# Kernel tuning notes

Measured on AMD Instinct MI355X. Metric: run time of the kernel, lower is better.

## Reference

```python
import jax, jax.numpy as jnp
import numpy as np

B, S, D, K = 32, 1024, 256, 1024
DECAY = 0.99
EPS = 1e-05          # EMA laplace epsilon
LN_EPS = 1e-05       # LayerNorm epsilon
COMMITMENT_COST = 0.25


def setup_inputs() -> dict:
    key = jax.random.key(0)
    k1, k2, k3 = jax.random.split(key, 3)
    inputs = jax.random.normal(k1, (B, S, D), jnp.float32)
    # nn.Embedding init: uniform(-1/K, 1/K)
    weight = jax.random.uniform(k2, (K, D), jnp.float32, -1.0 / K, 1.0 / K)
    ema_w = jax.random.normal(k3, (K, D), jnp.float32)
    ema_cluster_size = jnp.zeros((K,), jnp.float32)
    ln_gamma = jnp.ones((D,), jnp.float32)
    ln_beta = jnp.zeros((D,), jnp.float32)
    return {"inputs": inputs, "weight": weight, "ema_w": ema_w,
            "ema_cluster_size": ema_cluster_size,
            "ln_gamma": ln_gamma, "ln_beta": ln_beta}


def _layernorm(x, g, b):
    mu = jnp.mean(x, axis=-1, keepdims=True)
    var = jnp.mean((x - mu) ** 2, axis=-1, keepdims=True)
    return (x - mu) * jax.lax.rsqrt(var + LN_EPS) * g + b


def reference(inputs, weight, ema_w, ema_cluster_size, ln_gamma, ln_beta):
    flat_input = inputs.reshape(-1, D)          # [N, D] (unnormalized, used for EMA dw)
    feats = _layernorm(flat_input, ln_gamma, ln_beta)  # norm_input in sample()

    # euclidean distances ||f||^2 + ||w||^2 - 2 f w^T  -> [N, K]
    d = (jnp.sum(feats ** 2, axis=1, keepdims=True)
         + jnp.sum(weight ** 2, axis=1)
         - 2.0 * feats @ weight.T)

    sampled_dist = jnp.min(d, axis=1)           # [N]
    idx_flat = jnp.argmin(d, axis=1)            # [N] int

    # faithful reproduction of the source's reordering:
    # argsort per batch row (values in [0,S)) then flat-index into the [N]-long index vector
    order = jnp.argsort(sampled_dist.reshape(B, S), axis=1).reshape(-1)  # [N], values in [0,S)
    enc_idx = idx_flat[order]                   # [N]

    quantized = weight[enc_idx].reshape(B, S, D)

    # ---- EMA codebook update (training path), no gradients ----
    fi = jax.lax.stop_gradient(flat_input)
    counts = jax.ops.segment_sum(jnp.ones((B * S,), jnp.float32), enc_idx,
                                 num_segments=K)                    # encodings.sum(0)
    new_cs = ema_cluster_size * DECAY + (1.0 - DECAY) * counts
    n = jnp.sum(new_cs)
    new_cs = (new_cs + EPS) / (n + K * EPS) * n
    dw = jax.ops.segment_sum(fi, enc_idx, num_segments=K)            # encodings.T @ flat_input
    new_ema_w = jax.lax.stop_gradient(ema_w) * DECAY + (1.0 - DECAY) * dw
    new_weight = new_ema_w / new_cs[:, None]

    # ---- losses (avg=False, loss_type=0) ----
    e_latent = jnp.mean((jax.lax.stop_gradient(quantized) - inputs) ** 2)
    q_latent = jnp.mean((quantized - jax.lax.stop_gradient(inputs)) ** 2)
    loss = q_latent + COMMITMENT_COST * e_latent

    # straight-through estimator
    quantized_st = inputs + jax.lax.stop_gradient(quantized - inputs)

    avg_probs = counts / (B * S)
    perplexity = jnp.exp(-jnp.sum(avg_probs * jnp.log(avg_probs + 1e-10)))

    return quantized_st, loss, perplexity, enc_idx, new_weight, new_ema_w, new_cs
```

## Files before the change

### kernel.cpp

```cpp
#include <hip/hip_runtime.h>
#include <cmath>

#define B_ 32
#define S_ 1024
#define D_ 256
#define K_ 1024
#define N_ (B_*S_)

#define O_Q     0
#define O_LOSS  8388608
#define O_PERP  8388609
#define O_IDX   8388610
#define O_NW    8421378
#define O_NEW   8683522
#define O_NCS   8945666

#define OFF_FH    0ull
#define OFF_WH    16777216ull
#define OFF_BW    17301504ull
#define OFF_BWF   17309696ull
#define OFF_SAMP  17313792ull
#define OFF_IDXF  17575936ull
#define OFF_ENC   17707008ull
#define OFF_CNT   17838080ull
#define OFF_SLOWC 17842176ull
#define OFF_SLOWL 17842240ull
#define OFF_LOSSP 17973312ull
#define OFF_COFF  18235456ull
#define OFF_CUR   18239552ull
#define OFF_ROWL  18243648ull

#define MARGIN 4e-5f

typedef _Float16 f16x8 __attribute__((ext_vector_type(8)));
typedef float    f32x4 __attribute__((ext_vector_type(4)));

#define GL16(gp, lp) __builtin_amdgcn_global_load_lds( \
    (const __attribute__((address_space(1))) unsigned int*)(const void*)(gp), \
    (__attribute__((address_space(3))) unsigned int*)(void*)(lp), 16, 0, 0)

__global__ void k_pre(const float* __restrict__ x, const float* __restrict__ gam,
                      const float* __restrict__ bet, _Float16* __restrict__ fh,
                      const float* __restrict__ w, double* __restrict__ Bw,
                      float* __restrict__ Bwf, _Float16* __restrict__ wh) {
    int lane = threadIdx.x & 63, wv = threadIdx.x >> 6;
    if (blockIdx.x < N_ / 4) {
        int n = blockIdx.x * 4 + wv;
        const float* row = x + (size_t)n * D_;
        double xv[4], gv[4], bv[4];
#pragma unroll
        for (int i = 0; i < 4; i++) {
            int d = lane + 64 * i;
            xv[i] = row[d]; gv[i] = gam[d]; bv[i] = bet[d];
        }
        double s = xv[0] + xv[1] + xv[2] + xv[3];
        for (int m = 32; m > 0; m >>= 1) s += __shfl_xor(s, m, 64);
        double mu = s / 256.0, vs = 0.0;
#pragma unroll
        for (int i = 0; i < 4; i++) { double c = xv[i] - mu; vs += c * c; }
        for (int m = 32; m > 0; m >>= 1) vs += __shfl_xor(vs, m, 64);
        double inv = 1.0 / sqrt(vs / 256.0 + 1e-5);
#pragma unroll
        for (int i = 0; i < 4; i++) {
            int d = lane + 64 * i;
            float ff = (float)((xv[i] - mu) * inv * gv[i] + bv[i]);
            fh[(size_t)n * D_ + d] = (_Float16)ff;
        }
    } else {
        int k = (blockIdx.x - N_ / 4) * 4 + wv;
        double s = 0.0;
#pragma unroll
        for (int i = 0; i < 4; i++) {
            int d = lane + 64 * i;
            float v = w[(size_t)k * D_ + d];
            s += (double)v * (double)v;
            wh[(size_t)k * D_ + d] = (_Float16)v;
        }
        for (int m = 32; m > 0; m >>= 1) s += __shfl_xor(s, m, 64);
        if (lane == 0) { Bw[k] = s; Bwf[k] = (float)s; }
    }
}

__launch_bounds__(512, 4)
__global__ void k_phase1(const _Float16* __restrict__ fh, const _Float16* __restrict__ wh,
                         const float* __restrict__ Bwf, float* __restrict__ pq) {
    __shared__ __align__(16) _Float16 sA[3][128][32];
    __shared__ __align__(16) _Float16 sB[3][256][32];

    const int tid = threadIdx.x;
    const int lane = tid & 63;
    const int w = tid >> 6;
    const int wr = w >> 2;
    const int wc = w & 3;
    const int l15 = lane & 15;
    const int g = lane >> 4;
    const int id = blockIdx.x;
    const int grp = (id & 7) * 32 + (id >> 5);
    const int chunk = (id >> 3) & 3;
    const int row0 = grp * 128;
    const int c0 = chunk * 256;

    const int srow = lane >> 2;
    const int scol = (lane & 3) * 8;
    const _Float16* gp[3];
    int lrow[3]; int isA[3];
#pragma unroll
    for (int j = 0; j < 3; j++) {
        int li = w * 3 + j;
        if (li < 8) {
            isA[j] = 1; lrow[j] = li * 16;
            gp[j] = fh + (size_t)(row0 + li * 16 + srow) * 256 + scol;
        } else {
            isA[j] = 0; lrow[j] = (li - 8) * 16;
            gp[j] = wh + (size_t)(c0 + (li - 8) * 16 + srow) * 256 + scol;
        }
    }

    f32x4 acc[4][4];
#pragma unroll
    for (int a = 0; a < 4; a++)
#pragma unroll
        for (int b = 0; b < 4; b++) acc[a][b] = (f32x4){0.f, 0.f, 0.f, 0.f};

#define STAGE(bi, kk) do { \
    const int eoff_ = (kk) * 32; \
    _Pragma("unroll") \
    for (int j_ = 0; j_ < 3; j_++) { \
        if (isA[j_]) GL16(gp[j_] + eoff_, &sA[bi][lrow[j_]][0]); \
        else         GL16(gp[j_] + eoff_, &sB[bi][lrow[j_]][0]); \
    } \
} while (0)

    STAGE(0, 0);
    STAGE(1, 1);
    asm volatile("s_waitcnt vmcnt(3)" ::: "memory");
    __builtin_amdgcn_s_barrier();
    __builtin_amdgcn_sched_barrier(0);

#pragma unroll
    for (int ks = 0; ks < 8; ks++) {
        const int cur = ks % 3;
        if (ks < 6) STAGE((ks + 2) % 3, ks + 2);

        f16x8 bfr[4];
#pragma unroll
        for (int fc = 0; fc < 4; fc++)
            bfr[fc] = *(const f16x8*)&sB[cur][wc * 64 + fc * 16 + l15][g * 8];
        __builtin_amdgcn_s_setprio(1);
#pragma unroll
        for (int fr = 0; fr < 4; fr++) {
            f16x8 af = *(const f16x8*)&sA[cur][wr * 64 + fr * 16 + l15][g * 8];
#pragma unroll
            for (int fc = 0; fc < 4; fc++)
                acc[fr][fc] = __builtin_amdgcn_mfma_f32_16x16x32_f16(
                    af, bfr[fc], acc[fr][fc], 0, 0, 0);
        }
        __builtin_amdgcn_s_setprio(0);
        __builtin_amdgcn_sched_barrier(0);

        if (ks < 6)       asm volatile("s_waitcnt vmcnt(3)" ::: "memory");
        else if (ks == 6) asm volatile("s_waitcnt vmcnt(0)" ::: "memory");
        if (ks < 7) {
            __builtin_amdgcn_s_barrier();
            __builtin_amdgcn_sched_barrier(0);
        }
    }
#undef STAGE
    __syncthreads();

    float bwv[4];
#pragma unroll
    for (int fc = 0; fc < 4; fc++) bwv[fc] = Bwf[c0 + wc * 64 + fc * 16 + l15];
    float* red = (float*)&sA[0][0][0];
#pragma unroll
    for (int fr = 0; fr < 4; fr++) {
#pragma unroll
        for (int r = 0; r < 4; r++) {
            float m1 = 3e38f, m2 = 3e38f; int c1 = 0x7fffffff;
#pragma unroll
            for (int fc = 0; fc < 4; fc++) {
                float sv = fmaf(-2.0f, acc[fr][fc][r], bwv[fc]);
                int c = c0 + wc * 64 + fc * 16 + l15;
                if (sv < m1 || (sv == m1 && c < c1)) { m2 = m1; m1 = sv; c1 = c; }
                else if (sv < m2) m2 = sv;
            }
#pragma unroll
            for (int msk = 1; msk <= 8; msk <<= 1) {
                float om1 = __shfl_xor(m1, msk, 64);
                float om2 = __shfl_xor(m2, msk, 64);
                int   oc  = __shfl_xor(c1, msk, 64);
                if (om1 < m1 || (om1 == m1 && oc < c1)) {
                    m2 = (m1 < om2) ? m1 : om2; m1 = om1; c1 = oc;
                } else {
                    m2 = (om1 < m2) ? om1 : m2;
                }
            }
            if (l15 == 0) {
                int rl = wr * 64 + fr * 16 + g * 4 + r;
                int base = (rl * 4 + wc) * 3;
                red[base] = m1; red[base + 1] = m2; ((int*)red)[base + 2] = c1;
            }
        }
    }
    __syncthreads();
    if (tid < 128) {
        float M1 = 3e38f, M2 = 3e38f; int C1 = 0x7fffffff;
        for (int q = 0; q < 4; q++) {
            int base = (tid * 4 + q) * 3;
            float m1 = red[base], m2 = red[base + 1]; int c = ((int*)red)[base + 2];
            if (m1 < M1 || (m1 == M1 && c < C1)) {
                M2 = (M1 < m2) ? M1 : m2; M1 = m1; C1 = c;
            } else {
                M2 = (m1 < M2) ? m1 : M2;
            }
        }
        pq[chunk * N_ + row0 + tid] = M1;
        pq[4 * N_ + chunk * N_ + row0 + tid] = M2;
        ((int*)pq)[8 * N_ + chunk * N_ + row0 + tid] = C1;
    }
}

__global__ void k_phase2(const float* __restrict__ x, const float* __restrict__ gam,
                         const float* __restrict__ bet, const float* __restrict__ w,
                         const double* __restrict__ Bw, const float* __restrict__ pq,
                         double* __restrict__ sampled, int* __restrict__ idxf,
                         unsigned* __restrict__ slowC, int* __restrict__ slowL) {
    int lane = threadIdx.x & 63, wv = threadIdx.x >> 6;
    int n = blockIdx.x * 4 + wv;
    const float* pm1 = pq;
    const float* pm2 = pq + 4 * N_;
    const int*   pc1 = (const int*)pq + 8 * N_;
    float M1 = 3e38f, M2 = 3e38f; int C1 = 0x7fffffff;
#pragma unroll
    for (int c = 0; c < 4; c++) {
        float m1 = pm1[c * N_ + n], m2 = pm2[c * N_ + n]; int cc = pc1[c * N_ + n];
        if (m1 < M1 || (m1 == M1 && cc < C1)) {
            M2 = (M1 < m2) ? M1 : m2; M1 = m1; C1 = cc;
        } else {
            M2 = (m1 < M2) ? m1 : M2;
        }
    }
    if (M2 - M1 <= MARGIN) {
        if (lane == 0) { unsigned p = atomicAdd(slowC, 1u); slowL[p] = n; }
        return;
    }
    const float* row = x + (size_t)n * D_;
    double xv[4], gv[4], bv[4];
#pragma unroll
    for (int i = 0; i < 4; i++) {
        int d = lane + 64 * i;
        xv[i] = row[d]; gv[i] = gam[d]; bv[i] = bet[d];
    }
    double s = xv[0] + xv[1] + xv[2] + xv[3];
    for (int m = 32; m > 0; m >>= 1) s += __shfl_xor(s, m, 64);
    double mu = s / 256.0, vs = 0.0;
#pragma unroll
    for (int i = 0; i < 4; i++) { double c = xv[i] - mu; vs += c * c; }
    for (int m = 32; m > 0; m >>= 1) vs += __shfl_xor(vs, m, 64);
    double inv = 1.0 / sqrt(vs / 256.0 + 1e-5);
    double f[4], A = 0.0;
#pragma unroll
    for (int i = 0; i < 4; i++) {
        f[i] = (xv[i] - mu) * inv * gv[i] + bv[i];
        A += f[i] * f[i];
    }
    for (int m = 32; m > 0; m >>= 1) A += __shfl_xor(A, m, 64);

    const float* wr_ = w + (size_t)C1 * D_;
    double ss = 0.0;
#pragma unroll
    for (int i = 0; i < 4; i++) ss += f[i] * (double)wr_[lane + 64 * i];
    for (int m = 32; m > 0; m >>= 1) ss += __shfl_xor(ss, m, 64);
    if (lane == 0) { sampled[n] = (A + Bw[C1]) - 2.0 * ss; idxf[n] = C1; }
}

__launch_bounds__(256)
__global__ void k_slow(const float* __restrict__ x, const float* __restrict__ gam,
                       const float* __restrict__ bet, const float* __restrict__ w,
                       const double* __restrict__ Bw,
                       const int* __restrict__ slowL, const unsigned* __restrict__ slowC,
                       double* __restrict__ sampled, int* __restrict__ idxf) {
    __shared__ double sf[256];
    __shared__ double red8[8];
    __shared__ double bmW[4];
    __shared__ int    bcW[4];
    int tid = threadIdx.x, lane = tid & 63, wv = tid >> 6;
    int cnt = (int)*slowC;
    for (int it = blockIdx.x; it < cnt; it += gridDim.x) {
        int n = slowL[it];
        double xv = x[(size_t)n * D_ + tid];
        double gv = gam[tid], bv = bet[tid];
        double s = xv;
        for (int m = 32; m > 0; m >>= 1) s += __shfl_xor(s, m, 64);
        if (lane == 0) red8[wv] = s;
        __syncthreads();
        double mu = (red8[0] + red8[1] + red8[2] + red8[3]) / 256.0;
        double c = xv - mu;
        double v2 = c * c;
        for (int m = 32; m > 0; m >>= 1) v2 += __shfl_xor(v2, m, 64);
        __syncthreads();
        if (lane == 0) red8[wv] = v2;
        __syncthreads();
        double var = (red8[0] + red8[1] + red8[2] + red8[3]) / 256.0;
        double inv = 1.0 / sqrt(var + 1e-5);
        double f = c * inv * gv + bv;
        double a2 = f * f;
        for (int m = 32; m > 0; m >>= 1) a2 += __shfl_xor(a2, m, 64);
        if (lane == 0) red8[4 + wv] = a2;
        sf[tid] = f;
        __syncthreads();
        double A = red8[4] + red8[5] + red8[6] + red8[7];

        double bm = 1.0e300; int bc = 0x7fffffff;
        for (int r = 0; r < 4; r++) {
            int cc = r * 256 + wv * 64 + lane;
            const float* wr = w + (size_t)cc * D_;
            double acc = 0.0;
#pragma unroll 8
            for (int d4 = 0; d4 < 64; d4++) {
                float4 w4 = *(const float4*)(wr + d4 * 4);
                acc += sf[d4 * 4] * (double)w4.x + sf[d4 * 4 + 1] * (double)w4.y
                     + sf[d4 * 4 + 2] * (double)w4.z + sf[d4 * 4 + 3] * (double)w4.w;
            }
            double dist = (A + Bw[cc]) - 2.0 * acc;
            if (dist < bm) { bm = dist; bc = cc; }
        }
        for (int m = 32; m > 0; m >>= 1) {
            double om = __shfl_xor(bm, m, 64);
            int    oc = __shfl_xor(bc, m, 64);
            if (om < bm || (om == bm && oc < bc)) { bm = om; bc = oc; }
        }
        if (lane == 0) { bmW[wv] = bm; bcW[wv] = bc; }
        __syncthreads();
        if (tid == 0) {
            double M = bmW[0]; int C = bcW[0];
            for (int i = 1; i < 4; i++)
                if (bmW[i] < M || (bmW[i] == M && bcW[i] < C)) { M = bmW[i]; C = bcW[i]; }
            sampled[n] = M; idxf[n] = C;
        }
        __syncthreads();
    }
}

__launch_bounds__(1024)
__global__ void k_sort(const double* __restrict__ sampled, const int* __restrict__ idxf,
                       int* __restrict__ enc) {
    __shared__ double val[1024];
    __shared__ int    sid[1024];
    int b = blockIdx.x, t = threadIdx.x;
    val[t] = sampled[(size_t)b * S_ + t];
    sid[t] = t;
    __syncthreads();
    for (int k = 2; k <= 1024; k <<= 1) {
        for (int j = k >> 1; j > 0; j >>= 1) {
            int p = t ^ j;
            if (p > t) {
                double v0 = val[t], v1 = val[p];
                int i0 = sid[t], i1 = sid[p];
                bool gtv = (v0 > v1) || (v0 == v1 && i0 > i1);
                bool asc = ((t & k) == 0);
                if (asc ? gtv : !gtv) {
                    val[t] = v1; val[p] = v0; sid[t] = i1; sid[p] = i0;
                }
            }
            __syncthreads();
        }
    }
    enc[(size_t)b * S_ + t] = idxf[sid[t]];
}

__global__ void k_gather(const float* __restrict__ x, const float* __restrict__ w,
                         const int* __restrict__ enc, float* __restrict__ out,
                         unsigned* __restrict__ cnt, double* __restrict__ lossP) {
    int lane = threadIdx.x & 63, wv = threadIdx.x >> 6;
    int n = blockIdx.x * 4 + wv;
    int e = enc[n];
    const float* wr_ = w + (size_t)e * D_;
    const float* xr = x + (size_t)n * D_;
    float* qr = out + O_Q + (size_t)n * D_;
    double ls = 0.0;
#pragma unroll
    for (int i = 0; i < 4; i++) {
        int d = lane + 64 * i;
        float q = wr_[d], xv = xr[d];
        qr[d] = q;
        double df = (double)q - (double)xv;
        ls += df * df;
    }
    for (int m = 32; m > 0; m >>= 1) ls += __shfl_xor(ls, m, 64);
    if (lane == 0) {
        lossP[n] = ls;
        out[O_IDX + n] = (float)e;
        atomicAdd(&cnt[e], 1u);
    }
}

__launch_bounds__(1024)
__global__ void k_scan(const unsigned* __restrict__ cnt, int* __restrict__ coff,
                       int* __restrict__ cur) {
    __shared__ int tmp[1024];
    int t = threadIdx.x;
    int my = (int)cnt[t];
    tmp[t] = my;
    __syncthreads();
    for (int off = 1; off < 1024; off <<= 1) {
        int v = (t >= off) ? tmp[t - off] : 0;
        __syncthreads();
        tmp[t] += v;
        __syncthreads();
    }
    int excl = tmp[t] - my;
    coff[t] = excl;
    cur[t] = excl;
}

__global__ void k_scatter(const int* __restrict__ enc, int* __restrict__ cur,
                          int* __restrict__ rowl) {
    int n = blockIdx.x * 256 + threadIdx.x;
    int e = enc[n];
    int p = atomicAdd(&cur[e], 1);
    rowl[p] = n;
}

__launch_bounds__(256)
__global__ void k_post(const unsigned* __restrict__ cnt, const float* __restrict__ ema_cs,
                       const double* __restrict__ lossP,
                       const int* __restrict__ coff, const int* __restrict__ rowl,
                       const float* __restrict__ x, const float* __restrict__ ema_w,
                       float* __restrict__ out) {
    __shared__ double redd[24];
    __shared__ double ntot_s;
    int tid = threadIdx.x;

    double part = 0.0;
    for (int i = tid; i < K_; i += 256)
        part += (double)(0.99f * ema_cs[i] + 0.01f * (float)cnt[i]);
    for (int m = 32; m > 0; m >>= 1) part += __shfl_xor(part, m, 64);
    if ((tid & 63) == 0) redd[tid >> 6] = part;
    __syncthreads();
    if (tid == 0) ntot_s = redd[0] + redd[1] + redd[2] + redd[3];
    __syncthreads();
    double ntot = ntot_s;

    if (blockIdx.x < K_) {
        int k = blockIdx.x;
        float cs0 = 0.99f * ema_cs[k] + 0.01f * (float)cnt[k];
        double csf = ((double)cs0 + 1e-5) / (ntot + 1024.0 * 1e-5) * ntot;
        int base = coff[k];
        int c = (int)cnt[k];
        float acc = 0.0f;
        int j = 0;
        for (; j + 4 <= c; j += 4) {
            int r0 = rowl[base + j];
            int r1 = rowl[base + j + 1];
            int r2 = rowl[base + j + 2];
            int r3 = rowl[base + j + 3];
            float v0 = x[(size_t)r0 * D_ + tid];
            float v1 = x[(size_t)r1 * D_ + tid];
            float v2 = x[(size_t)r2 * D_ + tid];
            float v3 = x[(size_t)r3 * D_ + tid];
            acc += v0; acc += v1; acc += v2; acc += v3;
        }
        for (; j < c; j++) acc += x[(size_t)rowl[base + j] * D_ + tid];
        size_t idx = (size_t)k * D_ + tid;
        float ne = 0.99f * ema_w[idx] + 0.01f * acc;
        out[O_NEW + idx] = ne;
        out[O_NW + idx] = ne / (float)csf;
    } else {
        for (int i = tid; i < K_; i += 256) {
            float cs0 = 0.99f * ema_cs[i] + 0.01f * (float)cnt[i];
            double c2 = ((double)cs0 + 1e-5) / (ntot + 1024.0 * 1e-5) * ntot;
            out[O_NCS + i] = (float)c2;
        }
        double ent = 0.0;
        for (int i = tid; i < K_; i += 256) {
            double p = (double)cnt[i] / 32768.0;
            ent += -p * log(p + 1e-10);
        }
        for (int m = 32; m > 0; m >>= 1) ent += __shfl_xor(ent, m, 64);
        if ((tid & 63) == 0) redd[8 + (tid >> 6)] = ent;
        double ls = 0.0;
        for (int i = tid; i < N_; i += 256) ls += lossP[i];
        for (int m = 32; m > 0; m >>= 1) ls += __shfl_xor(ls, m, 64);
        if ((tid & 63) == 0) redd[16 + (tid >> 6)] = ls;
        __syncthreads();
        if (tid == 0) {
            double e = redd[8] + redd[9] + redd[10] + redd[11];
            double l = redd[16] + redd[17] + redd[18] + redd[19];
            out[O_PERP] = (float)exp(e);
            out[O_LOSS] = (float)(1.25 * l / 8388608.0);
        }
    }
}

extern "C" void kernel_launch(void* const* d_in, const int* in_sizes, int n_in,
                              void* d_out, int out_size, void* d_ws, size_t ws_size,
                              hipStream_t stream) {
    (void)in_sizes; (void)n_in; (void)out_size; (void)ws_size;
    const float* x      = (const float*)d_in[0];
    const float* w      = (const float*)d_in[1];
    const float* ema_w  = (const float*)d_in[2];
    const float* ema_cs = (const float*)d_in[3];
    const float* g      = (const float*)d_in[4];
    const float* bt     = (const float*)d_in[5];
    float* out = (float*)d_out;
    char* ws = (char*)d_ws;

    _Float16* fh = (_Float16*)(ws + OFF_FH);
    _Float16* wh = (_Float16*)(ws + OFF_WH);
    double* Bw   = (double*)(ws + OFF_BW);
    float*  Bwf  = (float*)(ws + OFF_BWF);
    double* samp = (double*)(ws + OFF_SAMP);
    int*    idxf = (int*)(ws + OFF_IDXF);
    int*    enc  = (int*)(ws + OFF_ENC);
    unsigned* cnt = (unsigned*)(ws + OFF_CNT);
    unsigned* slowC = (unsigned*)(ws + OFF_SLOWC);
    int*    slowL = (int*)(ws + OFF_SLOWL);
    double* lossP = (double*)(ws + OFF_LOSSP);
    int*    coff  = (int*)(ws + OFF_COFF);
    int*    cur   = (int*)(ws + OFF_CUR);
    int*    rowl  = (int*)(ws + OFF_ROWL);

    (void)hipMemsetAsync(ws + OFF_CNT, 0, 4160, stream);

    k_pre<<<N_ / 4 + K_ / 4, 256, 0, stream>>>(x, g, bt, fh, w, Bw, Bwf, wh);
    k_phase1<<<1024, 512, 0, stream>>>(fh, wh, Bwf, out);
    k_phase2<<<N_ / 4, 256, 0, stream>>>(x, g, bt, w, Bw, out, samp, idxf, slowC, slowL);
    k_slow<<<2048, 256, 0, stream>>>(x, g, bt, w, Bw, slowL, slowC, samp, idxf);
    k_sort<<<B_, 1024, 0, stream>>>(samp, idxf, enc);
    k_gather<<<N_ / 4, 256, 0, stream>>>(x, w, enc, out, cnt, lossP);
    k_scan<<<1, 1024, 0, stream>>>(cnt, coff, cur);
    k_scatter<<<N_ / 256, 256, 0, stream>>>(enc, cur, rowl);
    k_post<<<K_ + 1, 256, 0, stream>>>(cnt, ema_cs, lossP, coff, rowl, x, ema_w, out);
}
```

Baseline: 294.8 us.

## Vectorize pre/gather kernels, use float LayerNorm, transpose MFMA accumulators for argmin

The LayerNorm pre-kernel and the gather kernel now use float4 loads and stores, and LayerNorm is computed in float instead of double. The codebook-squared-norm path keeps double accumulation. In the distance GEMM the MFMA operands are swapped so each lane holds four consecutive codebook columns for a single row. The per-row min/second-min is then reduced mostly inside registers, needing 2 cross-lane shuffle steps instead of 4 per row. Float LayerNorm can shift near-tie argmin choices relative to the double version.

```diff
diff --git a/kernel.cpp b/kernel.cpp
--- a/kernel.cpp
+++ b/kernel.cpp
@@ -33,6 +33,7 @@
 #define MARGIN 4e-5f
 
 typedef _Float16 f16x8 __attribute__((ext_vector_type(8)));
+typedef _Float16 f16x4 __attribute__((ext_vector_type(4)));
 typedef float    f32x4 __attribute__((ext_vector_type(4)));
 
 #define GL16(gp, lp) __builtin_amdgcn_global_load_lds( \
@@ -46,37 +47,32 @@
     int lane = threadIdx.x & 63, wv = threadIdx.x >> 6;
     if (blockIdx.x < N_ / 4) {
         int n = blockIdx.x * 4 + wv;
-        const float* row = x + (size_t)n * D_;
-        double xv[4], gv[4], bv[4];
-#pragma unroll
-        for (int i = 0; i < 4; i++) {
-            int d = lane + 64 * i;
-            xv[i] = row[d]; gv[i] = gam[d]; bv[i] = bet[d];
-        }
-        double s = xv[0] + xv[1] + xv[2] + xv[3];
+        const float4 xv = ((const float4*)(x + (size_t)n * D_))[lane];
+        const float4 gv = ((const float4*)gam)[lane];
+        const float4 bv = ((const float4*)bet)[lane];
+        float s = xv.x + xv.y + xv.z + xv.w;
         for (int m = 32; m > 0; m >>= 1) s += __shfl_xor(s, m, 64);
-        double mu = s / 256.0, vs = 0.0;
-#pragma unroll
-        for (int i = 0; i < 4; i++) { double c = xv[i] - mu; vs += c * c; }
+        float mu = s * (1.0f / 256.0f);
+        float c0 = xv.x - mu, c1 = xv.y - mu, c2 = xv.z - mu, c3 = xv.w - mu;
+        float vs = c0 * c0 + c1 * c1 + c2 * c2 + c3 * c3;
         for (int m = 32; m > 0; m >>= 1) vs += __shfl_xor(vs, m, 64);
-        double inv = 1.0 / sqrt(vs / 256.0 + 1e-5);
-#pragma unroll
-        for (int i = 0; i < 4; i++) {
-            int d = lane + 64 * i;
-            float ff = (float)((xv[i] - mu) * inv * gv[i] + bv[i]);
-            fh[(size_t)n * D_ + d] = (_Float16)ff;
-        }
+        float inv = 1.0f / sqrtf(vs * (1.0f / 256.0f) + 1e-5f);
+        f16x4 o;
+        o[0] = (_Float16)(c0 * inv * gv.x + bv.x);
+        o[1] = (_Float16)(c1 * inv * gv.y + bv.y);
+        o[2] = (_Float16)(c2 * inv * gv.z + bv.z);
+        o[3] = (_Float16)(c3 * inv * gv.w + bv.w);
+        *(f16x4*)&fh[(size_t)n * D_ + lane * 4] = o;
     } else {
         int k = (blockIdx.x - N_ / 4) * 4 + wv;
-        double s = 0.0;
-#pragma unroll
-        for (int i = 0; i < 4; i++) {
-            int d = lane + 64 * i;
-            float v = w[(size_t)k * D_ + d];
-            s += (double)v * (double)v;
-            wh[(size_t)k * D_ + d] = (_Float16)v;
-        }
+        const float4 v = ((const float4*)(w + (size_t)k * D_))[lane];
+        double s = (double)v.x * v.x + (double)v.y * v.y
+                 + (double)v.z * v.z + (double)v.w * v.w;
         for (int m = 32; m > 0; m >>= 1) s += __shfl_xor(s, m, 64);
+        f16x4 o;
+        o[0] = (_Float16)v.x; o[1] = (_Float16)v.y;
+        o[2] = (_Float16)v.z; o[3] = (_Float16)v.w;
+        *(f16x4*)&wh[(size_t)k * D_ + lane * 4] = o;
         if (lane == 0) { Bw[k] = s; Bwf[k] = (float)s; }
     }
 }
@@ -142,18 +138,18 @@
         const int cur = ks % 3;
         if (ks < 6) STAGE((ks + 2) % 3, ks + 2);
 
-        f16x8 bfr[4];
-#pragma unroll
-        for (int fc = 0; fc < 4; fc++)
-            bfr[fc] = *(const f16x8*)&sB[cur][wc * 64 + fc * 16 + l15][g * 8];
+        f16x8 cfr[4];
+#pragma unroll
+        for (int cb = 0; cb < 4; cb++)
+            cfr[cb] = *(const f16x8*)&sB[cur][wc * 64 + cb * 16 + l15][g * 8];
         __builtin_amdgcn_s_setprio(1);
 #pragma unroll
-        for (int fr = 0; fr < 4; fr++) {
-            f16x8 af = *(const f16x8*)&sA[cur][wr * 64 + fr * 16 + l15][g * 8];
-#pragma unroll
-            for (int fc = 0; fc < 4; fc++)
-                acc[fr][fc] = __builtin_amdgcn_mfma_f32_16x16x32_f16(
-                    af, bfr[fc], acc[fr][fc], 0, 0, 0);
+        for (int rb = 0; rb < 4; rb++) {
+            f16x8 rf = *(const f16x8*)&sA[cur][wr * 64 + rb * 16 + l15][g * 8];
+#pragma unroll
+            for (int cb = 0; cb < 4; cb++)
+                acc[cb][rb] = __builtin_amdgcn_mfma_f32_16x16x32_f16(
+                    cfr[cb], rf, acc[cb][rb], 0, 0, 0);
         }
         __builtin_amdgcn_s_setprio(0);
         __builtin_amdgcn_sched_barrier(0);
@@ -168,38 +164,42 @@
 #undef STAGE
     __syncthreads();
 
-    float bwv[4];
-#pragma unroll
-    for (int fc = 0; fc < 4; fc++) bwv[fc] = Bwf[c0 + wc * 64 + fc * 16 + l15];
+    float bwv[4][4];
+#pragma unroll
+    for (int cb = 0; cb < 4; cb++)
+#pragma unroll
+        for (int r = 0; r < 4; r++)
+            bwv[cb][r] = Bwf[c0 + wc * 64 + cb * 16 + g * 4 + r];
+
     float* red = (float*)&sA[0][0][0];
 #pragma unroll
-    for (int fr = 0; fr < 4; fr++) {
-#pragma unroll
-        for (int r = 0; r < 4; r++) {
-            float m1 = 3e38f, m2 = 3e38f; int c1 = 0x7fffffff;
-#pragma unroll
-            for (int fc = 0; fc < 4; fc++) {
-                float sv = fmaf(-2.0f, acc[fr][fc][r], bwv[fc]);
-                int c = c0 + wc * 64 + fc * 16 + l15;
+    for (int rb = 0; rb < 4; rb++) {
+        float m1 = 3e38f, m2 = 3e38f; int c1 = 0x7fffffff;
+#pragma unroll
+        for (int cb = 0; cb < 4; cb++) {
+#pragma unroll
+            for (int r = 0; r < 4; r++) {
+                float sv = fmaf(-2.0f, acc[cb][rb][r], bwv[cb][r]);
+                int c = c0 + wc * 64 + cb * 16 + g * 4 + r;
                 if (sv < m1 || (sv == m1 && c < c1)) { m2 = m1; m1 = sv; c1 = c; }
                 else if (sv < m2) m2 = sv;
             }
-#pragma unroll
-            for (int msk = 1; msk <= 8; msk <<= 1) {
-                float om1 = __shfl_xor(m1, msk, 64);
-                float om2 = __shfl_xor(m2, msk, 64);
-                int   oc  = __shfl_xor(c1, msk, 64);
-                if (om1 < m1 || (om1 == m1 && oc < c1)) {
-                    m2 = (m1 < om2) ? m1 : om2; m1 = om1; c1 = oc;
-                } else {
-                    m2 = (om1 < m2) ? om1 : m2;
-                }
+        }
+#pragma unroll
+        for (int msk = 16; msk <= 32; msk <<= 1) {
+            float om1 = __shfl_xor(m1, msk, 64);
+            float om2 = __shfl_xor(m2, msk, 64);
+            int   oc  = __shfl_xor(c1, msk, 64);
+            if (om1 < m1 || (om1 == m1 && oc < c1)) {
+                m2 = (m1 < om2) ? m1 : om2; m1 = om1; c1 = oc;
+            } else {
+                m2 = (om1 < m2) ? om1 : m2;
             }
-            if (l15 == 0) {
-                int rl = wr * 64 + fr * 16 + g * 4 + r;
-                int base = (rl * 4 + wc) * 3;
-                red[base] = m1; red[base + 1] = m2; ((int*)red)[base + 2] = c1;
-            }
+        }
+        if (lane < 16) {
+            int rl = wr * 64 + rb * 16 + l15;
+            int base = (rl * 4 + wc) * 3;
+            red[base] = m1; red[base + 1] = m2; ((int*)red)[base + 2] = c1;
         }
     }
     __syncthreads();
@@ -375,18 +375,14 @@
     int lane = threadIdx.x & 63, wv = threadIdx.x >> 6;
     int n = blockIdx.x * 4 + wv;
     int e = enc[n];
-    const float* wr_ = w + (size_t)e * D_;
-    const float* xr = x + (size_t)n * D_;
-    float* qr = out + O_Q + (size_t)n * D_;
-    double ls = 0.0;
-#pragma unroll
-    for (int i = 0; i < 4; i++) {
-        int d = lane + 64 * i;
-        float q = wr_[d], xv = xr[d];
-        qr[d] = q;
-        double df = (double)q - (double)xv;
-        ls += df * df;
-    }
+    const float4 q4 = ((const float4*)(w + (size_t)e * D_))[lane];
+    const float4 x4 = ((const float4*)(x + (size_t)n * D_))[lane];
+    ((float4*)(out + O_Q + (size_t)n * D_))[lane] = q4;
+    double d0 = (double)q4.x - (double)x4.x;
+    double d1 = (double)q4.y - (double)x4.y;
+    double d2 = (double)q4.z - (double)x4.z;
+    double d3 = (double)q4.w - (double)x4.w;
+    double ls = d0 * d0 + d1 * d1 + d2 * d2 + d3 * d3;
     for (int m = 32; m > 0; m >>= 1) ls += __shfl_xor(ls, m, 64);
     if (lane == 0) {
         lossP[n] = ls;
```

Measured after the change: 272.7 us. 1.08x faster.
